# Kernel tuning notes

Hardware: AMD Instinct MI355X
Metric: run time of the kernel (lower is better)

The kernel has to match this reference:

```python
import jax, jax.numpy as jnp
import numpy as np

K = 11
EPS = 1e-6


def _box_sum(a):
    # a: [B, H, W] -> KxK zero-padded local sum (equivalent to nn.Unfold padding=K//2 then sum)
    return jax.lax.reduce_window(a, 0.0, jax.lax.add,
                                 window_dimensions=(1, K, K),
                                 window_strides=(1, 1, 1),
                                 padding='SAME')


def setup_inputs() -> dict:
    key = jax.random.key(0)
    k1, k2 = jax.random.split(key)
    x = jax.random.normal(k1, (8, 3, 1024, 1024), dtype=jnp.float32)
    y = jax.random.normal(k2, (8, 3, 1024, 1024), dtype=jnp.float32)
    return {"x": x, "y": y}


def reference(x, y):
    # Channel-reduce first, then local KxK box sums (math-identical to the
    # unfold-based sum over (C, K, K) with zero padding).
    xx = _box_sum((x * x).sum(axis=1))   # [B, H, W]
    yy = _box_sum((y * y).sum(axis=1))
    xy = _box_sum((x * y).sum(axis=1))
    x_norm = jnp.sqrt(xx)
    y_norm = jnp.sqrt(yy)
    return xy / (x_norm * y_norm + EPS)
```

## Files before the change

### kernel.cpp

```cpp
#include <hip/hip_runtime.h>
#include <math.h>

#define NB 8
#define NC 3
#define NH 1024
#define NW 1024
#define EPS 1e-6f

#define BAND 128
#define CH 32
#define KSTEPS (CH + 10)
#define PADW 144
#define NLD 36

__global__ __launch_bounds__(64, 2)
void lcs_kernel(const float* __restrict__ x, const float* __restrict__ y,
                float* __restrict__ out) {
    __shared__ __align__(16) float P[2][3][PADW];

    const int l   = threadIdx.x;
    const int bid = blockIdx.x;
    const int b     = bid >> 8;
    const int rem   = bid & 255;
    const int band0 = (rem & 7) * BAND;
    const int r0    = (rem >> 3) * CH;

    const size_t chan = (size_t)NH * NW;
    const float* xb = x + (size_t)b * NC * chan;
    const float* yb = y + (size_t)b * NC * chan;

    const int c0 = band0 - 8 + 4 * l;
    const bool lv = (l < NLD) && (c0 >= 0) && (c0 + 3 <= NW - 1);
    const float cm = lv ? 1.f : 0.f;
    const int oc = lv ? c0 : 0;

    float4 cur[6], nx1[6], nx2[6];
    auto ldrow = [&](int gr, float4* d) {
        const int rc = gr < 0 ? 0 : (gr > NH - 1 ? NH - 1 : gr);
        const size_t ro = (size_t)rc * NW;
        if (l < NLD) {
            #pragma unroll
            for (int c = 0; c < 3; ++c) {
                d[c]     = *(const float4*)(xb + c * chan + ro + oc);
                d[3 + c] = *(const float4*)(yb + c * chan + ro + oc);
            }
        }
    };

    ldrow(r0 - 5, cur);
    ldrow(r0 - 4, nx1);

    float2 ring[3][11];
    #pragma unroll
    for (int p = 0; p < 3; ++p)
        #pragma unroll
        for (int s = 0; s < 11; ++s) ring[p][s] = make_float2(0.f, 0.f);
    float2 vs[3] = {make_float2(0.f,0.f), make_float2(0.f,0.f), make_float2(0.f,0.f)};

    for (int g = 0; g < 4; ++g) {
        const int gg = g & 1;
        #pragma unroll
        for (int s = 0; s < 11; ++s) {
            const int k = g * 11 + s;
            if (k >= KSTEPS) continue;

            if (k + 2 < KSTEPS) ldrow(r0 - 3 + k, nx2);

            const int gr = r0 - 5 + k;
            const float rmf = (gr >= 0 && gr < NH) ? 1.f : 0.f;
            const float cmr = rmf * cm;

            float4 pxx = make_float4(0.f,0.f,0.f,0.f), pyy = pxx, pxy = pxx;
            #pragma unroll
            for (int c = 0; c < 3; ++c) {
                const float4 fx = cur[c], fy = cur[3 + c];
                pxx.x += fx.x*fx.x; pxx.y += fx.y*fx.y; pxx.z += fx.z*fx.z; pxx.w += fx.w*fx.w;
                pyy.x += fy.x*fy.x; pyy.y += fy.y*fy.y; pyy.z += fy.z*fy.z; pyy.w += fy.w*fy.w;
                pxy.x += fx.x*fy.x; pxy.y += fx.y*fy.y; pxy.z += fx.z*fy.z; pxy.w += fx.w*fy.w;
            }
            pxx.x *= cmr; pxx.y *= cmr; pxx.z *= cmr; pxx.w *= cmr;
            pyy.x *= cmr; pyy.y *= cmr; pyy.z *= cmr; pyy.w *= cmr;
            pxy.x *= cmr; pxy.y *= cmr; pxy.z *= cmr; pxy.w *= cmr;

            const int pp = gg ^ (s & 1);
            float* Pb = &P[pp][0][0];

            if (l < NLD) {
                *(float4*)(Pb + 0*PADW + 4*l) = pxx;
                *(float4*)(Pb + 1*PADW + 4*l) = pyy;
                *(float4*)(Pb + 2*PADW + 4*l) = pxy;
            }
            __builtin_amdgcn_wave_barrier();

            #pragma unroll
            for (int p = 0; p < 3; ++p) {
                const float* Pq = Pb + p * PADW;
                float2 t[7];
                #pragma unroll
                for (int j = 0; j < 7; ++j)
                    t[j] = *(const float2*)(Pq + 2*l + 2 + 2*j);
                float h0 = ((t[0].y + t[1].x) + (t[1].y + t[2].x))
                         + ((t[2].y + t[3].x) + (t[3].y + t[4].x))
                         + ((t[4].y + t[5].x) + t[5].y);
                float h1 = h0 - t[0].y + t[6].x;
                vs[p].x += h0 - ring[p][s].x;
                vs[p].y += h1 - ring[p][s].y;
                ring[p][s].x = h0;
                ring[p][s].y = h1;
            }

            if (k >= 10) {
                const int orow = r0 + k - 10;
                const float d0 = __builtin_amdgcn_sqrtf(vs[0].x) *
                                 __builtin_amdgcn_sqrtf(vs[1].x) + EPS;
                const float d1 = __builtin_amdgcn_sqrtf(vs[0].y) *
                                 __builtin_amdgcn_sqrtf(vs[1].y) + EPS;
                float2 o;
                o.x = vs[2].x * __builtin_amdgcn_rcpf(d0);
                o.y = vs[2].y * __builtin_amdgcn_rcpf(d1);
                *(float2*)(out + ((size_t)b * NH + orow) * NW + band0 + 2*l) = o;
            }

            if (k + 1 < KSTEPS) {
                #pragma unroll
                for (int i = 0; i < 6; ++i) { cur[i] = nx1[i]; nx1[i] = nx2[i]; }
            }
        }
    }
}

extern "C" void kernel_launch(void* const* d_in, const int* in_sizes, int n_in,
                              void* d_out, int out_size, void* d_ws, size_t ws_size,
                              hipStream_t stream) {
    const float* x = (const float*)d_in[0];
    const float* y = (const float*)d_in[1];
    float* out = (float*)d_out;
    lcs_kernel<<<dim3(2048), dim3(64), 0, stream>>>(x, y, out);
}
```

Before: 256.5 us.

## Halve column band width to 64, use float2 loads and single-row prefetch

The column band per block shrinks from 128 to 64 output columns, which doubles the grid to 4096 single-wave blocks. Each lane now loads float2 per channel instead of float4, and the prefetch depth drops from two rows to one, cutting register pressure. Only 32 of 64 lanes produce output, and the 10-column halo becomes a larger share of each load, so redundant global reads and idle lanes increase in exchange for more parallelism.

```diff
diff --git a/kernel.cpp b/kernel.cpp
--- a/kernel.cpp
+++ b/kernel.cpp
@@ -7,11 +7,10 @@
 #define NW 1024
 #define EPS 1e-6f
 
-#define BAND 128
+#define BAND 64
 #define CH 32
 #define KSTEPS (CH + 10)
-#define PADW 144
-#define NLD 36
+#define PADW 160
 
 __global__ __launch_bounds__(64, 2)
 void lcs_kernel(const float* __restrict__ x, const float* __restrict__ y,
@@ -20,35 +19,31 @@
 
     const int l   = threadIdx.x;
     const int bid = blockIdx.x;
-    const int b     = bid >> 8;
-    const int rem   = bid & 255;
-    const int band0 = (rem & 7) * BAND;
-    const int r0    = (rem >> 3) * CH;
+    const int b     = bid >> 9;
+    const int rem   = bid & 511;
+    const int band0 = (rem & 15) * BAND;
+    const int r0    = (rem >> 4) * CH;
 
     const size_t chan = (size_t)NH * NW;
     const float* xb = x + (size_t)b * NC * chan;
     const float* yb = y + (size_t)b * NC * chan;
 
-    const int c0 = band0 - 8 + 4 * l;
-    const bool lv = (l < NLD) && (c0 >= 0) && (c0 + 3 <= NW - 1);
-    const float cm = lv ? 1.f : 0.f;
-    const int oc = lv ? c0 : 0;
+    const int gc0 = band0 - 8 + 2 * l;
+    const float cm = (l < 40 && gc0 >= 0 && gc0 + 1 <= NW - 1) ? 1.f : 0.f;
+    const int oc = gc0 < 0 ? 0 : (gc0 > NW - 2 ? NW - 2 : gc0);
 
-    float4 cur[6], nx1[6], nx2[6];
-    auto ldrow = [&](int gr, float4* d) {
+    float2 cur[6], nxt[6];
+    auto ldrow = [&](int gr, float2* d) {
         const int rc = gr < 0 ? 0 : (gr > NH - 1 ? NH - 1 : gr);
         const size_t ro = (size_t)rc * NW;
-        if (l < NLD) {
-            #pragma unroll
-            for (int c = 0; c < 3; ++c) {
-                d[c]     = *(const float4*)(xb + c * chan + ro + oc);
-                d[3 + c] = *(const float4*)(yb + c * chan + ro + oc);
-            }
+        #pragma unroll
+        for (int c = 0; c < 3; ++c) {
+            d[c]     = *(const float2*)(xb + c * chan + ro + oc);
+            d[3 + c] = *(const float2*)(yb + c * chan + ro + oc);
         }
     };
 
     ldrow(r0 - 5, cur);
-    ldrow(r0 - 4, nx1);
 
     float2 ring[3][11];
     #pragma unroll
@@ -64,31 +59,31 @@
             const int k = g * 11 + s;
             if (k >= KSTEPS) continue;
 
-            if (k + 2 < KSTEPS) ldrow(r0 - 3 + k, nx2);
+            if (k + 1 < KSTEPS) ldrow(r0 - 4 + k, nxt);
 
             const int gr = r0 - 5 + k;
             const float rmf = (gr >= 0 && gr < NH) ? 1.f : 0.f;
             const float cmr = rmf * cm;
 
-            float4 pxx = make_float4(0.f,0.f,0.f,0.f), pyy = pxx, pxy = pxx;
+            float2 pxx = make_float2(0.f,0.f), pyy = pxx, pxy = pxx;
             #pragma unroll
             for (int c = 0; c < 3; ++c) {
-                const float4 fx = cur[c], fy = cur[3 + c];
-                pxx.x += fx.x*fx.x; pxx.y += fx.y*fx.y; pxx.z += fx.z*fx.z; pxx.w += fx.w*fx.w;
-                pyy.x += fy.x*fy.x; pyy.y += fy.y*fy.y; pyy.z += fy.z*fy.z; pyy.w += fy.w*fy.w;
-                pxy.x += fx.x*fy.x; pxy.y += fx.y*fy.y; pxy.z += fx.z*fy.z; pxy.w += fx.w*fy.w;
+                const float2 fx = cur[c], fy = cur[3 + c];
+                pxx.x += fx.x*fx.x; pxx.y += fx.y*fx.y;
+                pyy.x += fy.x*fy.x; pyy.y += fy.y*fy.y;
+                pxy.x += fx.x*fy.x; pxy.y += fx.y*fy.y;
             }
-            pxx.x *= cmr; pxx.y *= cmr; pxx.z *= cmr; pxx.w *= cmr;
-            pyy.x *= cmr; pyy.y *= cmr; pyy.z *= cmr; pyy.w *= cmr;
-            pxy.x *= cmr; pxy.y *= cmr; pxy.z *= cmr; pxy.w *= cmr;
+            pxx.x *= cmr; pxx.y *= cmr;
+            pyy.x *= cmr; pyy.y *= cmr;
+            pxy.x *= cmr; pxy.y *= cmr;
 
             const int pp = gg ^ (s & 1);
             float* Pb = &P[pp][0][0];
 
-            if (l < NLD) {
-                *(float4*)(Pb + 0*PADW + 4*l) = pxx;
-                *(float4*)(Pb + 1*PADW + 4*l) = pyy;
-                *(float4*)(Pb + 2*PADW + 4*l) = pxy;
+            if (l < 40) {
+                *(float2*)(Pb + 0*PADW + 2*l) = pxx;
+                *(float2*)(Pb + 1*PADW + 2*l) = pyy;
+                *(float2*)(Pb + 2*PADW + 2*l) = pxy;
             }
             __builtin_amdgcn_wave_barrier();
 
@@ -109,7 +104,7 @@
                 ring[p][s].y = h1;
             }
 
-            if (k >= 10) {
+            if (k >= 10 && l < 32) {
                 const int orow = r0 + k - 10;
                 const float d0 = __builtin_amdgcn_sqrtf(vs[0].x) *
                                  __builtin_amdgcn_sqrtf(vs[1].x) + EPS;
@@ -123,7 +118,7 @@
 
             if (k + 1 < KSTEPS) {
                 #pragma unroll
-                for (int i = 0; i < 6; ++i) { cur[i] = nx1[i]; nx1[i] = nx2[i]; }
+                for (int i = 0; i < 6; ++i) cur[i] = nxt[i];
             }
         }
     }
@@ -135,5 +130,5 @@
     const float* x = (const float*)d_in[0];
     const float* y = (const float*)d_in[1];
     float* out = (float*)d_out;
-    lcs_kernel<<<dim3(2048), dim3(64), 0, stream>>>(x, y, out);
+    lcs_kernel<<<dim3(4096), dim3(64), 0, stream>>>(x, y, out);
 }
```

After: 255.5 us. Within noise of the previous version (-0.4%).
